# Kernel tuning notes

Measured on AMD Instinct MI355X. Metric: run time of the kernel, lower is better.

Reference implementation:

```python
import jax, jax.numpy as jnp
import numpy as np

PE_DIM = 40  # pe_dim; gaussian PE scale factor = pe_dim // 2


def _batched_linear(x, wb):
    # x: [B, N, D], wb: [B, D+1, H] (last row is bias)
    return jnp.einsum('bnd,bdh->bnh', x, wb[:, :-1, :]) + wb[:, -1:, :]


def setup_inputs() -> dict:
    key = jax.random.key(0)
    ks = jax.random.split(key, 8)
    B, N = 16, 16384
    H = 256
    pe_out = 3 * PE_DIM  # 120
    s = 0.05  # keep ReLU-chain activations bounded
    return {
        'x': jax.random.normal(ks[0], (B, N, 3), dtype=jnp.float32),
        'wb0': jax.random.normal(ks[1], (B, pe_out + 1, H), dtype=jnp.float32) * s,
        'wb1': jax.random.normal(ks[2], (B, H + 1, H), dtype=jnp.float32) * s,
        'wb2': jax.random.normal(ks[3], (B, H + 1, H), dtype=jnp.float32) * s,
        'wb3': jax.random.normal(ks[4], (B, H + 1, H), dtype=jnp.float32) * s,
        'wb4': jax.random.normal(ks[5], (B, H + 1, H), dtype=jnp.float32) * s,
        'wb_out': jax.random.normal(ks[6], (B, H + 1, 1), dtype=jnp.float32) * s,
        'rand_freqs': jax.random.normal(ks[7], (3 * (PE_DIM // 2), 3), dtype=jnp.float32),  # feat_sigma=1
    }


def reference(x, wb0, wb1, wb2, wb3, wb4, wb_out, rand_freqs):
    # Gaussian positional encoding: k = x . (rand_freqs * pe_dim//2)
    k = jnp.einsum('bnd,fd->bnf', x, rand_freqs * (PE_DIM // 2))  # [B,N,60]
    h = jnp.concatenate([jnp.sin(k), jnp.cos(k)], axis=-1)        # [B,N,120]
    for wb in (wb0, wb1, wb2, wb3, wb4):
        h = jax.nn.relu(_batched_linear(h, wb))
    out = _batched_linear(h, wb_out)  # [B,N,1]
    return out
```

## Files before the change

### kernel.cpp

```cpp
#include <hip/hip_runtime.h>
#include <hip/hip_bf16.h>


#define H 256
#define MT 64
#define PE_NF 60

typedef __attribute__((ext_vector_type(8))) short s16x8;
typedef __attribute__((ext_vector_type(4))) float f32x4;

#define BATCH_BYTES (size_t)589824
#define BATCH_ELEMS (size_t)294912

static __device__ __forceinline__ unsigned short f2bf(float v) {
  unsigned int u = __float_as_uint(v);
  return (unsigned short)((u + 0x7FFFu + ((u >> 16) & 1u)) >> 16);
}
static __device__ __forceinline__ int hswz(int row, int chunk) {
  return (chunk & ~7) | ((chunk ^ row) & 7);
}

static __device__ __forceinline__ void bar_raw() {
  asm volatile("s_barrier" ::: "memory");
}
static __device__ __forceinline__ void bar_lgkm() {
  asm volatile("s_waitcnt lgkmcnt(0)\n\ts_barrier" ::: "memory");
}

__global__ __launch_bounds__(256) void prep_weights(
    const float* __restrict__ wb0, const float* __restrict__ wb1,
    const float* __restrict__ wb2, const float* __restrict__ wb3,
    const float* __restrict__ wb4,
    unsigned short* __restrict__ wpk, float* __restrict__ biases) {
  int z = blockIdx.z;
  int li = z >> 4, b = z & 15;
  int k0 = blockIdx.x * 32;
  int n0 = blockIdx.y * 32;
  int Ks;
  const float* src;
  unsigned short* dst;
  if (li == 0) {
    Ks = 120;
    if (k0 >= 128) return;
    src = wb0 + (size_t)b * 121 * H;
    dst = wpk + b * BATCH_ELEMS;
  } else {
    Ks = 256;
    const float* srcs[4] = {wb1, wb2, wb3, wb4};
    src = srcs[li - 1] + (size_t)b * 257 * H;
    dst = wpk + b * BATCH_ELEMS + 32768 + (size_t)(li - 1) * 65536;
  }
  __shared__ float tile[32][33];
  int t = threadIdx.x;
  int tx = t & 31, ty = t >> 5;
#pragma unroll
  for (int i = 0; i < 4; ++i) {
    int k = k0 + ty + i * 8;
    tile[ty + i * 8][tx] = (k < Ks) ? src[(size_t)k * H + n0 + tx] : 0.f;
  }
  if (k0 == 0 && ty == 0)
    biases[((size_t)li * 16 + b) * H + n0 + tx] = src[(size_t)Ks * H + n0 + tx];
  __syncthreads();
  if (t < 128) {
    int nn = t & 31, kg = t >> 5;
    int n = n0 + nn;
    int kt = k0 >> 5;
    union { unsigned short us[8]; s16x8 v; } pk;
#pragma unroll
    for (int j = 0; j < 8; ++j) pk.us[j] = f2bf(tile[kg * 8 + j][nn]);
    *(s16x8*)&dst[(size_t)(kt * 16 + (n >> 4)) * 512 + (kg * 16 + (n & 15)) * 8] = pk.v;
  }
}

template <int NKT, bool LAST>
static __device__ __forceinline__ void mlp_layer(
    const char*& fp, const float* __restrict__ bl,
    unsigned short* __restrict__ h_s, const float* __restrict__ wout_s,
    const int rlane, const int kgrp, const int wc, const int l,
    s16x8 (&wf)[2][4], float* psum) {
  static_assert((NKT & 1) == 0, "parity needs even NKT");
  f32x4 acc[4][4];
#pragma unroll
  for (int ct = 0; ct < 4; ++ct) {
    f32x4 bini = *(const f32x4*)(bl + wc * 64 + ct * 16 + kgrp * 4);
#pragma unroll
    for (int rt = 0; rt < 4; ++rt) acc[rt][ct] = bini;
  }

  const char* hb = (const char*)h_s;
  const unsigned be = rlane * 512 + hswz(rlane, kgrp) * 16;
  const unsigned bo = rlane * 512 + hswz(rlane, 4 + kgrp) * 16;

#pragma unroll
  for (int kt = 0; kt < NKT; ++kt) {
    s16x8 af[4];
    const unsigned base = ((kt & 1) ? bo : be) + (kt >> 1) * 128;
#pragma unroll
    for (int rt = 0; rt < 4; ++rt)
      af[rt] = *(const s16x8*)(hb + base + rt * 8192);

    if (!(LAST && kt == NKT - 1)) {
#pragma unroll
      for (int c = 0; c < 4; ++c)
        wf[(kt + 1) & 1][c] = *(const s16x8*)(fp + c * 1024);
      fp += 16384;
    }
    __builtin_amdgcn_s_setprio(1);
#pragma unroll
    for (int rt = 0; rt < 4; ++rt)
#pragma unroll
      for (int ct = 0; ct < 4; ++ct)
        acc[rt][ct] = __builtin_amdgcn_mfma_f32_16x16x32_bf16(
            wf[kt & 1][ct], af[rt], acc[rt][ct], 0, 0, 0);
    __builtin_amdgcn_s_setprio(0);
  }

  if constexpr (LAST) {
    float p[4];
#pragma unroll
    for (int rt = 0; rt < 4; ++rt) {
      float s = 0.f;
#pragma unroll
      for (int ct = 0; ct < 4; ++ct) {
        f32x4 wv = *(const f32x4*)(wout_s + wc * 64 + ct * 16 + kgrp * 4);
#pragma unroll
        for (int g = 0; g < 4; ++g)
          s += fmaxf(acc[rt][ct][g], 0.f) * wv[g];
      }
      s += __shfl_xor(s, 16);
      s += __shfl_xor(s, 32);
      p[rt] = s;
    }
    if (l < 16) {
#pragma unroll
      for (int rt = 0; rt < 4; ++rt)
        psum[wc * 64 + rt * 16 + l] = p[rt];
    }
  } else {
    bar_raw();
    const int sub = (kgrp & 1) * 4;
    const int cbase = wc * 8 + (kgrp >> 1);
#pragma unroll
    for (int rt = 0; rt < 4; ++rt) {
      const int m = rt * 16 + rlane;
      const int rowb = m * 256;
#pragma unroll
      for (int ct = 0; ct < 4; ++ct) {
        const int cs = hswz(m, cbase + ct * 2);
        float v0 = fmaxf(acc[rt][ct][0], 0.f);
        float v1 = fmaxf(acc[rt][ct][1], 0.f);
        float v2 = fmaxf(acc[rt][ct][2], 0.f);
        float v3 = fmaxf(acc[rt][ct][3], 0.f);
        union { __hip_bfloat162 h2[2]; uint2 u; } pk;
        pk.h2[0] = __float22bfloat162_rn(float2{v0, v1});
        pk.h2[1] = __float22bfloat162_rn(float2{v2, v3});
        *(uint2*)&h_s[rowb + cs * 8 + sub] = pk.u;
      }
    }
    bar_lgkm();
  }
}

__global__ __launch_bounds__(256, 4) void hyponerf_main(
    const float* __restrict__ x, const float* __restrict__ rfreq,
    const float* __restrict__ wbout, const unsigned short* __restrict__ wpk,
    const float* __restrict__ biases, float* __restrict__ out) {
  __shared__ __align__(16) unsigned short h_s[MT * 256];
  __shared__ float fr_s[PE_NF * 3];
  __shared__ float x_s[MT * 3];
  __shared__ float wout_s[H + 1];
  __shared__ float psum[4 * 64];

  int bid = blockIdx.x;
  int logical = (bid & 7) * 512 + (bid >> 3);
  int b  = logical >> 8;
  int mt = logical & 255;

  int t = threadIdx.x;
  int wc = t >> 6, l = t & 63;
  int rlane = l & 15;
  int kgrp  = l >> 4;

  const char* fp = (const char*)wpk + b * BATCH_BYTES
                 + (size_t)wc * 4096 + (size_t)l * 16;

  s16x8 wf[2][4];
#pragma unroll
  for (int c = 0; c < 4; ++c) wf[0][c] = *(const s16x8*)(fp + c * 1024);
  fp += 16384;

  const float* xg = x + ((size_t)b * 16384 + (size_t)mt * MT) * 3;
  for (int i = t; i < MT * 3; i += 256) x_s[i] = xg[i];
  for (int i = t; i < PE_NF * 3; i += 256) fr_s[i] = rfreq[i] * 20.0f;
  for (int i = t; i < H + 1; i += 256) wout_s[i] = wbout[(size_t)b * (H + 1) + i];
  bar_lgkm();

  {
    int r = t >> 2;
    int q = t & 3;
    float x0 = x_s[r * 3 + 0], x1 = x_s[r * 3 + 1], x2 = x_s[r * 3 + 2];
    int rowb = r * 256;
#pragma unroll
    for (int cc = 0; cc < 4; ++cc) {
      int ch = q * 4 + cc;
      union { unsigned short us[8]; s16x8 v; } pk;
#pragma unroll
      for (int j = 0; j < 8; ++j) {
        int n = ch * 8 + j;
        float v = 0.f;
        if (n < 60) {
          float kv = x0 * fr_s[n * 3] + x1 * fr_s[n * 3 + 1] + x2 * fr_s[n * 3 + 2];
          v = __sinf(kv);
        } else if (n < 120) {
          int f = n - 60;
          float kv = x0 * fr_s[f * 3] + x1 * fr_s[f * 3 + 1] + x2 * fr_s[f * 3 + 2];
          v = __cosf(kv);
        }
        pk.us[j] = f2bf(v);
      }
      *(s16x8*)&h_s[rowb + hswz(r, ch) * 8] = pk.v;
    }
  }
  bar_lgkm();

  const float* bb = biases + (size_t)b * H;
  mlp_layer<4, false>(fp, bb + 0 * 16 * H, h_s, wout_s, rlane, kgrp, wc, l,
                      wf, psum);
  mlp_layer<8, false>(fp, bb + 1 * 16 * H, h_s, wout_s, rlane, kgrp, wc, l,
                      wf, psum);
  mlp_layer<8, false>(fp, bb + 2 * 16 * H, h_s, wout_s, rlane, kgrp, wc, l,
                      wf, psum);
  mlp_layer<8, false>(fp, bb + 3 * 16 * H, h_s, wout_s, rlane, kgrp, wc, l,
                      wf, psum);
  mlp_layer<8, true >(fp, bb + 4 * 16 * H, h_s, wout_s, rlane, kgrp, wc, l,
                      wf, psum);

  bar_lgkm();
  if (t < MT) {
    float s = psum[t] + psum[64 + t] + psum[128 + t] + psum[192 + t];
    out[(size_t)b * 16384 + (size_t)mt * MT + t] = s + wout_s[H];
  }
}

extern "C" void kernel_launch(void* const* d_in, const int* in_sizes, int n_in,
                              void* d_out, int out_size, void* d_ws, size_t ws_size,
                              hipStream_t stream) {
  const float* x     = (const float*)d_in[0];
  const float* wb0   = (const float*)d_in[1];
  const float* wb1   = (const float*)d_in[2];
  const float* wb2   = (const float*)d_in[3];
  const float* wb3   = (const float*)d_in[4];
  const float* wb4   = (const float*)d_in[5];
  const float* wbout = (const float*)d_in[6];
  const float* rfreq = (const float*)d_in[7];
  float* out = (float*)d_out;

  char* ws = (char*)d_ws;
  unsigned short* wpk = (unsigned short*)ws;
  float* biases = (float*)(ws + 16 * BATCH_BYTES);

  prep_weights<<<dim3(8, 8, 80), 256, 0, stream>>>(wb0, wb1, wb2, wb3, wb4,
                                                   wpk, biases);
  hyponerf_main<<<dim3(4096), 256, 0, stream>>>(x, rfreq, wbout, wpk,
                                                biases, out);
}
```

Before: 174.8 us.

## Double-buffer LDS activation fragments and keep output weights in registers

Activation fragments for the next k-step are now read from shared memory one step ahead into a second register buffer, so LDS latency can overlap the current MFMA batch. The output-layer weights and bias move from shared memory into per-thread registers, and the shared staging array is dropped. Launch bounds fall from 4 to 3 blocks per CU to make room for the extra registers. This trades occupancy for software pipelining, and the last layer now issues one unused weight prefetch past the end of its data.

```diff
diff --git a/kernel.cpp b/kernel.cpp
--- a/kernel.cpp
+++ b/kernel.cpp
@@ -75,10 +75,10 @@
 template <int NKT, bool LAST>
 static __device__ __forceinline__ void mlp_layer(
     const char*& fp, const float* __restrict__ bl,
-    unsigned short* __restrict__ h_s, const float* __restrict__ wout_s,
+    unsigned short* __restrict__ h_s,
     const int rlane, const int kgrp, const int wc, const int l,
-    s16x8 (&wf)[2][4], float* psum) {
-  static_assert((NKT & 1) == 0, "parity needs even NKT");
+    s16x8 (&wf)[2][4], const float* wout_r, float* psum) {
+  static_assert((NKT & 1) == 0, "ping-pong parity needs even NKT");
   f32x4 acc[4][4];
 #pragma unroll
   for (int ct = 0; ct < 4; ++ct) {
@@ -91,19 +91,22 @@
   const unsigned be = rlane * 512 + hswz(rlane, kgrp) * 16;
   const unsigned bo = rlane * 512 + hswz(rlane, 4 + kgrp) * 16;
 
+  s16x8 af[2][4];
+#pragma unroll
+  for (int rt = 0; rt < 4; ++rt)
+    af[0][rt] = *(const s16x8*)(hb + be + rt * 8192);
+
 #pragma unroll
   for (int kt = 0; kt < NKT; ++kt) {
-    s16x8 af[4];
-    const unsigned base = ((kt & 1) ? bo : be) + (kt >> 1) * 128;
-#pragma unroll
-    for (int rt = 0; rt < 4; ++rt)
-      af[rt] = *(const s16x8*)(hb + base + rt * 8192);
-
-    if (!(LAST && kt == NKT - 1)) {
-#pragma unroll
-      for (int c = 0; c < 4; ++c)
-        wf[(kt + 1) & 1][c] = *(const s16x8*)(fp + c * 1024);
-      fp += 16384;
+#pragma unroll
+    for (int c = 0; c < 4; ++c)
+      wf[(kt + 1) & 1][c] = *(const s16x8*)(fp + c * 1024);
+    fp += 16384;
+    if (kt + 1 < NKT) {
+      const unsigned base = (((kt + 1) & 1) ? bo : be) + ((kt + 1) >> 1) * 128;
+#pragma unroll
+      for (int rt = 0; rt < 4; ++rt)
+        af[(kt + 1) & 1][rt] = *(const s16x8*)(hb + base + rt * 8192);
     }
     __builtin_amdgcn_s_setprio(1);
 #pragma unroll
@@ -111,7 +114,7 @@
 #pragma unroll
       for (int ct = 0; ct < 4; ++ct)
         acc[rt][ct] = __builtin_amdgcn_mfma_f32_16x16x32_bf16(
-            wf[kt & 1][ct], af[rt], acc[rt][ct], 0, 0, 0);
+            wf[kt & 1][ct], af[kt & 1][rt], acc[rt][ct], 0, 0, 0);
     __builtin_amdgcn_s_setprio(0);
   }
 
@@ -121,12 +124,10 @@
     for (int rt = 0; rt < 4; ++rt) {
       float s = 0.f;
 #pragma unroll
-      for (int ct = 0; ct < 4; ++ct) {
-        f32x4 wv = *(const f32x4*)(wout_s + wc * 64 + ct * 16 + kgrp * 4);
+      for (int ct = 0; ct < 4; ++ct)
 #pragma unroll
         for (int g = 0; g < 4; ++g)
-          s += fmaxf(acc[rt][ct][g], 0.f) * wv[g];
-      }
+          s += fmaxf(acc[rt][ct][g], 0.f) * wout_r[ct * 4 + g];
       s += __shfl_xor(s, 16);
       s += __shfl_xor(s, 32);
       p[rt] = s;
@@ -161,14 +162,13 @@
   }
 }
 
-__global__ __launch_bounds__(256, 4) void hyponerf_main(
+__global__ __launch_bounds__(256, 3) void hyponerf_main(
     const float* __restrict__ x, const float* __restrict__ rfreq,
     const float* __restrict__ wbout, const unsigned short* __restrict__ wpk,
     const float* __restrict__ biases, float* __restrict__ out) {
   __shared__ __align__(16) unsigned short h_s[MT * 256];
   __shared__ float fr_s[PE_NF * 3];
   __shared__ float x_s[MT * 3];
-  __shared__ float wout_s[H + 1];
   __shared__ float psum[4 * 64];
 
   int bid = blockIdx.x;
@@ -189,10 +189,19 @@
   for (int c = 0; c < 4; ++c) wf[0][c] = *(const s16x8*)(fp + c * 1024);
   fp += 16384;
 
+  float wout_r[16];
+  {
+    const float* wob = wbout + (size_t)b * (H + 1) + wc * 64 + kgrp * 4;
+#pragma unroll
+    for (int ct = 0; ct < 4; ++ct)
+#pragma unroll
+      for (int g = 0; g < 4; ++g) wout_r[ct * 4 + g] = wob[ct * 16 + g];
+  }
+  const float wout_bias = wbout[(size_t)b * (H + 1) + H];
+
   const float* xg = x + ((size_t)b * 16384 + (size_t)mt * MT) * 3;
   for (int i = t; i < MT * 3; i += 256) x_s[i] = xg[i];
   for (int i = t; i < PE_NF * 3; i += 256) fr_s[i] = rfreq[i] * 20.0f;
-  for (int i = t; i < H + 1; i += 256) wout_s[i] = wbout[(size_t)b * (H + 1) + i];
   bar_lgkm();
 
   {
@@ -224,21 +233,21 @@
   bar_lgkm();
 
   const float* bb = biases + (size_t)b * H;
-  mlp_layer<4, false>(fp, bb + 0 * 16 * H, h_s, wout_s, rlane, kgrp, wc, l,
-                      wf, psum);
-  mlp_layer<8, false>(fp, bb + 1 * 16 * H, h_s, wout_s, rlane, kgrp, wc, l,
-                      wf, psum);
-  mlp_layer<8, false>(fp, bb + 2 * 16 * H, h_s, wout_s, rlane, kgrp, wc, l,
-                      wf, psum);
-  mlp_layer<8, false>(fp, bb + 3 * 16 * H, h_s, wout_s, rlane, kgrp, wc, l,
-                      wf, psum);
-  mlp_layer<8, true >(fp, bb + 4 * 16 * H, h_s, wout_s, rlane, kgrp, wc, l,
-                      wf, psum);
+  mlp_layer<4, false>(fp, bb + 0 * 16 * H, h_s, rlane, kgrp, wc, l, wf,
+                      wout_r, psum);
+  mlp_layer<8, false>(fp, bb + 1 * 16 * H, h_s, rlane, kgrp, wc, l, wf,
+                      wout_r, psum);
+  mlp_layer<8, false>(fp, bb + 2 * 16 * H, h_s, rlane, kgrp, wc, l, wf,
+                      wout_r, psum);
+  mlp_layer<8, false>(fp, bb + 3 * 16 * H, h_s, rlane, kgrp, wc, l, wf,
+                      wout_r, psum);
+  mlp_layer<8, true >(fp, bb + 4 * 16 * H, h_s, rlane, kgrp, wc, l, wf,
+                      wout_r, psum);
 
   bar_lgkm();
   if (t < MT) {
     float s = psum[t] + psum[64 + t] + psum[128 + t] + psum[192 + t];
-    out[(size_t)b * 16384 + (size_t)mt * MT + t] = s + wout_s[H];
+    out[(size_t)b * 16384 + (size_t)mt * MT + t] = s + wout_bias;
   }
 }
 
```

Result: faster. 163.3 us (-6.6%).
